# Performance work log

Measured on AMD Instinct MI355X. Metric: run time of the kernel, lower is better.

Reference implementation:

```python
import jax, jax.numpy as jnp
import numpy as np

B, S, D, H, E, K = 2, 2048, 1024, 2048, 8, 2


def setup_inputs() -> dict:
    key = jax.random.key(0)
    ks = jax.random.split(key, 9)
    sc_d = 1.0 / np.sqrt(D)
    sc_h = 1.0 / np.sqrt(H)
    return {
        "x": jax.random.normal(ks[0], (B, S, D), dtype=jnp.float32),
        "w_router": jax.random.normal(ks[1], (E, D), dtype=jnp.float32) * sc_d,
        "Wg": jax.random.normal(ks[2], (E, H, D), dtype=jnp.float32) * sc_d,  # per-expert gate proj (torch Linear weight layout [out,in])
        "Wu": jax.random.normal(ks[3], (E, H, D), dtype=jnp.float32) * sc_d,
        "Wd": jax.random.normal(ks[4], (E, D, H), dtype=jnp.float32) * sc_h,
        "sg": jax.random.normal(ks[5], (H, D), dtype=jnp.float32) * sc_d,  # shared expert
        "su": jax.random.normal(ks[6], (H, D), dtype=jnp.float32) * sc_d,
        "sd": jax.random.normal(ks[7], (D, H), dtype=jnp.float32) * sc_h,
    }


def reference(x, w_router, Wg, Wu, Wd, sg, su, sd):
    b, s, d = x.shape
    xf = x.reshape(-1, d)  # [T, D]

    # --- gating ---
    logits = jnp.einsum("td,ed->te", xf, w_router)
    probs = jax.nn.softmax(logits, axis=-1)  # [T, E]
    topw, topi = jax.lax.top_k(probs, K)  # [T, K]
    topw = topw / jnp.sum(topw, axis=-1, keepdims=True)
    # combine weights per (token, expert): topk indices are distinct per token
    comb = jnp.sum(topw[..., None] * jax.nn.one_hot(topi, E, dtype=xf.dtype), axis=1)  # [T, E]

    # --- shared expert (SwiGLU) ---
    shared = jnp.einsum(
        "th,dh->td",
        jax.nn.silu(jnp.einsum("td,hd->th", xf, sg)) * jnp.einsum("td,hd->th", xf, su),
        sd,
    )

    # --- routed experts: dense all-expert compute, weighted combine ---
    h1 = jax.nn.silu(jnp.einsum("td,ehd->teh", xf, Wg))
    h2 = jnp.einsum("td,ehd->teh", xf, Wu)
    eo = jnp.einsum("teh,edh->ted", h1 * h2, Wd)  # [T, E, D]
    routed = jnp.einsum("te,ted->td", comb, eo)

    return (routed + shared).reshape(b, s, d)
```

## Files before the change

kernel.cpp:

```cpp
#include <hip/hip_runtime.h>
#include <hip/hip_bf16.h>

#define T_TOK 4096
#define D_DIM 1024
#define H_DIM 2048

typedef __attribute__((ext_vector_type(8))) short short8;
typedef __attribute__((ext_vector_type(8))) unsigned short ushort8;
typedef __attribute__((ext_vector_type(4))) float floatx4;

__device__ __forceinline__ unsigned short f2bf(float f) {
  unsigned int u = __builtin_bit_cast(unsigned int, f);
  return (unsigned short)((u + 0x7fffu + ((u >> 16) & 1u)) >> 16);
}

__device__ __forceinline__ float bf2f(unsigned short s) {
  unsigned int u = ((unsigned int)s) << 16;
  return __builtin_bit_cast(float, u);
}

__device__ __forceinline__ void glds16(const ushort* g, ushort* l) {
  __builtin_amdgcn_global_load_lds(
      (const __attribute__((address_space(1))) unsigned int*)g,
      (__attribute__((address_space(3))) unsigned int*)l, 16, 0, 0);
}

__global__ void prep_kernel(const float4* __restrict__ Wg, ushort4* __restrict__ Wgb,
                            const float4* __restrict__ Wu, ushort4* __restrict__ Wub,
                            const float4* __restrict__ Wd, ushort4* __restrict__ Wdb,
                            const float4* __restrict__ sg, ushort4* __restrict__ sgb,
                            const float4* __restrict__ su, ushort4* __restrict__ sub,
                            const float4* __restrict__ sd, ushort4* __restrict__ sdb,
                            const float* __restrict__ x, const float* __restrict__ wr,
                            ushort* __restrict__ xb,
                            int* __restrict__ topi, float2* __restrict__ topw) {
  if (blockIdx.x < 27648) {
    int i2 = (blockIdx.x * 256 + threadIdx.x) * 2;
    const float4* s; ushort4* d; int i;
    if (i2 < 4194304)       { s = Wg; d = Wgb; i = i2; }
    else if (i2 < 8388608)  { s = Wu; d = Wub; i = i2 - 4194304; }
    else if (i2 < 12582912) { s = Wd; d = Wdb; i = i2 - 8388608; }
    else if (i2 < 13107200) { s = sg; d = sgb; i = i2 - 12582912; }
    else if (i2 < 13631488) { s = su; d = sub; i = i2 - 13107200; }
    else                    { s = sd; d = sdb; i = i2 - 13631488; }
    float4 v0 = s[i];
    float4 v1 = s[i + 1];
    ushort8 o;
    o[0] = f2bf(v0.x); o[1] = f2bf(v0.y); o[2] = f2bf(v0.z); o[3] = f2bf(v0.w);
    o[4] = f2bf(v1.x); o[5] = f2bf(v1.y); o[6] = f2bf(v1.z); o[7] = f2bf(v1.w);
    *(ushort8*)(d + i) = o;
    return;
  }
  const int w = threadIdx.x >> 6;
  const int l = threadIdx.x & 63;
  const int t = (blockIdx.x - 27648) * 4 + w;
  const float4* xr = (const float4*)(x + (size_t)t * D_DIM);
  ushort4* xo = (ushort4*)(xb + (size_t)t * D_DIM);
  float p[8];
#pragma unroll
  for (int e = 0; e < 8; ++e) p[e] = 0.f;
#pragma unroll
  for (int i = 0; i < 4; ++i) {
    float4 xv = xr[i * 64 + l];
    ushort4 o;
    o.x = f2bf(xv.x); o.y = f2bf(xv.y); o.z = f2bf(xv.z); o.w = f2bf(xv.w);
    xo[i * 64 + l] = o;
#pragma unroll
    for (int e = 0; e < 8; ++e) {
      float4 wv = ((const float4*)(wr + e * D_DIM))[i * 64 + l];
      p[e] += xv.x * wv.x + xv.y * wv.y + xv.z * wv.z + xv.w * wv.w;
    }
  }
#pragma unroll
  for (int off = 32; off > 0; off >>= 1) {
#pragma unroll
    for (int e = 0; e < 8; ++e) p[e] += __shfl_xor(p[e], off, 64);
  }
  if (l == 0) {
    float mx = p[0];
#pragma unroll
    for (int e = 1; e < 8; ++e) mx = fmaxf(mx, p[e]);
    float pr[8];
#pragma unroll
    for (int e = 0; e < 8; ++e) pr[e] = __expf(p[e] - mx);
    int i0 = 0;
#pragma unroll
    for (int e = 1; e < 8; ++e) if (pr[e] > pr[i0]) i0 = e;
    int i1 = (i0 == 0) ? 1 : 0;
#pragma unroll
    for (int e = 0; e < 8; ++e) if (e != i0 && pr[e] > pr[i1]) i1 = e;
    float w0 = pr[i0], w1 = pr[i1];
    float inv = 1.f / (w0 + w1);
    topi[t] = i0 | (i1 << 8);
    topw[t] = make_float2(w0 * inv, w1 * inv);
  }
}

__global__ void build_lists_kernel(const int* __restrict__ topi,
                                   int* __restrict__ counts, int* __restrict__ list,
                                   int* __restrict__ pos) {
  const int e = blockIdx.x;
  const int tid = threadIdx.x;
  const int l = tid & 63;
  const int w = tid >> 6;
  __shared__ int wtot[4];
  int base = 0;
  for (int c = 0; c < T_TOK; c += 256) {
    int t = c + tid;
    int ti = topi[t];
    int e0 = ti & 255, e1 = ti >> 8;
    bool flag = (e0 == e) || (e1 == e);
    unsigned long long m = __ballot(flag);
    int lanepos = __popcll(m & ((1ull << l) - 1ull));
    if (l == 0) wtot[w] = __popcll(m);
    __syncthreads();
    int waveoff = 0;
#pragma unroll
    for (int i = 0; i < 4; ++i) waveoff += (i < w) ? wtot[i] : 0;
    int tot = wtot[0] + wtot[1] + wtot[2] + wtot[3];
    if (flag) {
      int p = base + waveoff + lanepos;
      list[e * T_TOK + p] = t;
      int slot = (e0 == e) ? 0 : 1;
      pos[t * 2 + slot] = p;
    }
    base += tot;
    __syncthreads();
  }
  if (tid == 0) counts[e] = base;
}

__global__ __launch_bounds__(256, 2)
void gemm1_kernel(const ushort* __restrict__ xb,
                  const ushort* __restrict__ Wgb, const ushort* __restrict__ Wub,
                  const ushort* __restrict__ sgb, const ushort* __restrict__ sub,
                  const int* __restrict__ list, const int* __restrict__ counts,
                  ushort* __restrict__ h) {
  const int e = blockIdx.z;
  int n_e, hbase;
  {
    int acc = 0, ce = 0;
    for (int q = 0; q < 8; ++q) {
      int c = counts[q];
      if (q < e) acc += c;
      if (q == e) ce = c;
    }
    n_e = (e == 8) ? T_TOK : ce;
    hbase = (e == 8) ? 8192 : acc;
  }
  const int r0 = blockIdx.y * 128;
  if (r0 >= n_e) return;
  const int c0 = blockIdx.x * 128;
  const ushort* Wg = (e == 8) ? sgb : (Wgb + (size_t)e * H_DIM * D_DIM);
  const ushort* Wu = (e == 8) ? sub : (Wub + (size_t)e * H_DIM * D_DIM);
  const int hrow0 = hbase + r0;

  __shared__ __align__(16) ushort As[128 * 64];
  __shared__ __align__(16) ushort Bgs[128 * 64];
  __shared__ __align__(16) ushort Bus[128 * 64];
  __shared__ int toks[128];

  const int tid = threadIdx.x;
  const int l = tid & 63;
  const int w = tid >> 6;

  if (tid < 128) {
    int rr = r0 + tid;
    toks[tid] = (e == 8) ? ((rr < T_TOK) ? rr : (T_TOK - 1))
                         : list[e * T_TOK + ((rr < n_e) ? rr : (n_e - 1))];
  }
  __syncthreads();

  const int lrow8 = l >> 3;
  const int csw = (((l & 7) ^ lrow8) << 3);
  const ushort* ap[4];
#pragma unroll
  for (int i = 0; i < 4; ++i) {
    int ri = (w * 4 + i) * 8 + lrow8;
    ap[i] = xb + (size_t)toks[ri] * D_DIM + csw;
  }
  const ushort* bgp = Wg + (size_t)(c0 + w * 32 + lrow8) * D_DIM + csw;
  const ushort* bup = Wu + (size_t)(c0 + w * 32 + lrow8) * D_DIM + csw;

  floatx4 accg[4][4], accu[4][4];
#pragma unroll
  for (int i = 0; i < 4; ++i)
#pragma unroll
    for (int j = 0; j < 4; ++j) {
      accg[i][j] = (floatx4)(0.f);
      accu[i][j] = (floatx4)(0.f);
    }

  const int mrow = (w & 1) * 64;
  const int ncol = (w >> 1) * 64;
  int rba[4], rbb[4];
#pragma unroll
  for (int i = 0; i < 4; ++i) {
    rba[i] = (mrow + 16 * i + (l & 15)) * 64;
    rbb[i] = (ncol + 16 * i + (l & 15)) * 64;
  }

  for (int k0 = 0; k0 < D_DIM; k0 += 64) {
    __syncthreads();
#pragma unroll
    for (int i = 0; i < 4; ++i) {
      glds16(ap[i] + k0,                As  + (w * 4 + i) * 512);
      glds16(bgp + k0 + i * 8 * D_DIM,  Bgs + (w * 4 + i) * 512);
      glds16(bup + k0 + i * 8 * D_DIM,  Bus + (w * 4 + i) * 512);
    }
    __syncthreads();
#pragma unroll
    for (int s = 0; s < 2; ++s) {
      const int pq = ((((s << 2) | (l >> 4)) ^ (l & 7)) << 3);
      short8 a[4], bg[4], bu[4];
#pragma unroll
      for (int i = 0; i < 4; ++i) a[i] = *(const short8*)(As + rba[i] + pq);
#pragma unroll
      for (int j = 0; j < 4; ++j) {
        bg[j] = *(const short8*)(Bgs + rbb[j] + pq);
        bu[j] = *(const short8*)(Bus + rbb[j] + pq);
      }
#pragma unroll
      for (int i = 0; i < 4; ++i)
#pragma unroll
        for (int j = 0; j < 4; ++j) {
          accg[i][j] = __builtin_amdgcn_mfma_f32_16x16x32_bf16(a[i], bg[j], accg[i][j], 0, 0, 0);
          accu[i][j] = __builtin_amdgcn_mfma_f32_16x16x32_bf16(a[i], bu[j], accu[i][j], 0, 0, 0);
        }
    }
  }

#pragma unroll
  for (int i = 0; i < 4; ++i) {
#pragma unroll
    for (int r = 0; r < 4; ++r) {
      int lrow = mrow + 16 * i + (l >> 4) * 4 + r;
      if (r0 + lrow < n_e) {
#pragma unroll
        for (int j = 0; j < 4; ++j) {
          float g = accg[i][j][r];
          float u = accu[i][j][r];
          float hv = (g / (1.f + __expf(-g))) * u;
          int col = c0 + ncol + 16 * j + (l & 15);
          h[(size_t)(hrow0 + lrow) * H_DIM + col] = f2bf(hv);
        }
      }
    }
  }
}

__global__ __launch_bounds__(256, 2)
void gemm2_kernel(const ushort* __restrict__ h,
                  const ushort* __restrict__ Wdb, const ushort* __restrict__ sdb,
                  const int* __restrict__ counts,
                  ushort* __restrict__ eo) {
  const int e = blockIdx.z;
  int n_e, hbase;
  {
    int acc = 0, ce = 0;
    for (int q = 0; q < 8; ++q) {
      int c = counts[q];
      if (q < e) acc += c;
      if (q == e) ce = c;
    }
    n_e = (e == 8) ? T_TOK : ce;
    hbase = (e == 8) ? 8192 : acc;
  }
  const int r0 = blockIdx.y * 128;
  if (r0 >= n_e) return;
  const int c0 = blockIdx.x * 256;
  const ushort* Wd = (e == 8) ? sdb : (Wdb + (size_t)e * D_DIM * H_DIM);
  const int hrow0 = hbase + r0;

  __shared__ __align__(16) ushort As[128 * 64];
  __shared__ __align__(16) ushort Bs[256 * 64];

  const int tid = threadIdx.x;
  const int l = tid & 63;
  const int w = tid >> 6;

  const int lrow8 = l >> 3;
  const int csw = (((l & 7) ^ lrow8) << 3);
  const ushort* apb = h  + (size_t)(hrow0 + w * 32 + lrow8) * H_DIM + csw;
  const ushort* bpb = Wd + (size_t)(c0 + w * 64 + lrow8) * H_DIM + csw;

  floatx4 acc[4][8];
#pragma unroll
  for (int i = 0; i < 4; ++i)
#pragma unroll
    for (int j = 0; j < 8; ++j) acc[i][j] = (floatx4)(0.f);

  const int mrow = (w & 1) * 64;
  const int ncol = (w >> 1) * 128;
  int rba[4], rbb[8];
#pragma unroll
  for (int i = 0; i < 4; ++i) rba[i] = (mrow + 16 * i + (l & 15)) * 64;
#pragma unroll
  for (int j = 0; j < 8; ++j) rbb[j] = (ncol + 16 * j + (l & 15)) * 64;

  for (int k0 = 0; k0 < H_DIM; k0 += 64) {
    __syncthreads();
#pragma unroll
    for (int i = 0; i < 4; ++i)
      glds16(apb + k0 + i * 8 * H_DIM, As + (w * 4 + i) * 512);
#pragma unroll
    for (int i = 0; i < 8; ++i)
      glds16(bpb + k0 + i * 8 * H_DIM, Bs + (w * 8 + i) * 512);
    __syncthreads();
#pragma unroll
    for (int s = 0; s < 2; ++s) {
      const int pq = ((((s << 2) | (l >> 4)) ^ (l & 7)) << 3);
      short8 a[4], b[8];
#pragma unroll
      for (int i = 0; i < 4; ++i) a[i] = *(const short8*)(As + rba[i] + pq);
#pragma unroll
      for (int j = 0; j < 8; ++j) b[j] = *(const short8*)(Bs + rbb[j] + pq);
#pragma unroll
      for (int i = 0; i < 4; ++i)
#pragma unroll
        for (int j = 0; j < 8; ++j)
          acc[i][j] = __builtin_amdgcn_mfma_f32_16x16x32_bf16(a[i], b[j], acc[i][j], 0, 0, 0);
    }
  }

#pragma unroll
  for (int i = 0; i < 4; ++i) {
#pragma unroll
    for (int r = 0; r < 4; ++r) {
      int lrow = mrow + 16 * i + (l >> 4) * 4 + r;
      if (r0 + lrow < n_e) {
#pragma unroll
        for (int j = 0; j < 8; ++j) {
          int col = c0 + ncol + 16 * j + (l & 15);
          eo[(size_t)(hrow0 + lrow) * D_DIM + col] = f2bf(acc[i][j][r]);
        }
      }
    }
  }
}

__global__ void combine_kernel(const ushort* __restrict__ eo, const int* __restrict__ topi,
                               const float2* __restrict__ topw, const int* __restrict__ pos,
                               const int* __restrict__ counts, float* __restrict__ out) {
  const int t = blockIdx.x * 2 + (threadIdx.x >> 7);
  const int c = threadIdx.x & 127;
  int ti = topi[t];
  int e0 = ti & 255, e1 = ti >> 8;
  int off0 = 0, off1 = 0;
#pragma unroll
  for (int q = 0; q < 8; ++q) {
    int cc = counts[q];
    off0 += (q < e0) ? cc : 0;
    off1 += (q < e1) ? cc : 0;
  }
  float2 wv = topw[t];
  int2 p = ((const int2*)pos)[t];
  const short8* ra = (const short8*)(eo + (size_t)(off0 + p.x) * D_DIM);
  const short8* rb = (const short8*)(eo + (size_t)(off1 + p.y) * D_DIM);
  const short8* rs = (const short8*)(eo + (size_t)(8192 + t) * D_DIM);
  short8 a = ra[c], b = rb[c], s = rs[c];
  float o[8];
#pragma unroll
  for (int j = 0; j < 8; ++j)
    o[j] = wv.x * bf2f((unsigned short)a[j]) + wv.y * bf2f((unsigned short)b[j]) +
           bf2f((unsigned short)s[j]);
  float4* op = (float4*)(out + (size_t)t * D_DIM + c * 8);
  op[0] = make_float4(o[0], o[1], o[2], o[3]);
  op[1] = make_float4(o[4], o[5], o[6], o[7]);
}

#define OFF_XB   0ull
#define OFF_WGB  (OFF_XB + 8388608ull)
#define OFF_WUB  (OFF_WGB + 33554432ull)
#define OFF_WDB  (OFF_WUB + 33554432ull)
#define OFF_SGB  (OFF_WDB + 33554432ull)
#define OFF_SUB  (OFF_SGB + 4194304ull)
#define OFF_SDB  (OFF_SUB + 4194304ull)
#define OFF_H    (OFF_SDB + 4194304ull)
#define OFF_EO   OFF_WGB
#define OFF_CNT  (OFF_H + 50331648ull)
#define OFF_LIST (OFF_CNT + 64ull)
#define OFF_POS  (OFF_LIST + 131072ull)
#define OFF_TOPI (OFF_POS + 32768ull)
#define OFF_TOPW (OFF_TOPI + 16384ull)

extern "C" void kernel_launch(void* const* d_in, const int* in_sizes, int n_in,
                              void* d_out, int out_size, void* d_ws, size_t ws_size,
                              hipStream_t stream) {
  const float* x  = (const float*)d_in[0];
  const float* wr = (const float*)d_in[1];
  const float* Wg = (const float*)d_in[2];
  const float* Wu = (const float*)d_in[3];
  const float* Wd = (const float*)d_in[4];
  const float* sg = (const float*)d_in[5];
  const float* su = (const float*)d_in[6];
  const float* sd = (const float*)d_in[7];
  float* out = (float*)d_out;
  char* ws = (char*)d_ws;

  ushort* xb  = (ushort*)(ws + OFF_XB);
  ushort* Wgb = (ushort*)(ws + OFF_WGB);
  ushort* Wub = (ushort*)(ws + OFF_WUB);
  ushort* Wdb = (ushort*)(ws + OFF_WDB);
  ushort* sgb = (ushort*)(ws + OFF_SGB);
  ushort* sub = (ushort*)(ws + OFF_SUB);
  ushort* sdb = (ushort*)(ws + OFF_SDB);
  ushort* hbuf = (ushort*)(ws + OFF_H);
  ushort* eo   = (ushort*)(ws + OFF_EO);
  int* counts = (int*)(ws + OFF_CNT);
  int* list   = (int*)(ws + OFF_LIST);
  int* pos    = (int*)(ws + OFF_POS);
  int* topi   = (int*)(ws + OFF_TOPI);
  float2* topw = (float2*)(ws + OFF_TOPW);

  prep_kernel<<<28672, 256, 0, stream>>>((const float4*)Wg, (ushort4*)Wgb,
                                         (const float4*)Wu, (ushort4*)Wub,
                                         (const float4*)Wd, (ushort4*)Wdb,
                                         (const float4*)sg, (ushort4*)sgb,
                                         (const float4*)su, (ushort4*)sub,
                                         (const float4*)sd, (ushort4*)sdb,
                                         x, wr, xb, topi, topw);
  build_lists_kernel<<<8, 256, 0, stream>>>(topi, counts, list, pos);

  gemm1_kernel<<<dim3(16, 32, 9), 256, 0, stream>>>(xb, Wgb, Wub, sgb, sub,
                                                    list, counts, hbuf);
  gemm2_kernel<<<dim3(4, 32, 9), 256, 0, stream>>>(hbuf, Wdb, sdb, counts, eo);
  combine_kernel<<<2048, 256, 0, stream>>>(eo, topi, topw, pos, counts, out);
}
```

Before: 452.8 us.

## Overlap Wd/sd bf16 conversion with gemm1 and shrink gemm2 tile width

```diff
diff --git a/kernel.cpp b/kernel.cpp
--- a/kernel.cpp
+++ b/kernel.cpp
@@ -27,22 +27,19 @@
 
 __global__ void prep_kernel(const float4* __restrict__ Wg, ushort4* __restrict__ Wgb,
                             const float4* __restrict__ Wu, ushort4* __restrict__ Wub,
-                            const float4* __restrict__ Wd, ushort4* __restrict__ Wdb,
                             const float4* __restrict__ sg, ushort4* __restrict__ sgb,
                             const float4* __restrict__ su, ushort4* __restrict__ sub,
-                            const float4* __restrict__ sd, ushort4* __restrict__ sdb,
                             const float* __restrict__ x, const float* __restrict__ wr,
                             ushort* __restrict__ xb,
                             int* __restrict__ topi, float2* __restrict__ topw) {
-  if (blockIdx.x < 27648) {
-    int i2 = (blockIdx.x * 256 + threadIdx.x) * 2;
-    const float4* s; ushort4* d; int i;
-    if (i2 < 4194304)       { s = Wg; d = Wgb; i = i2; }
-    else if (i2 < 8388608)  { s = Wu; d = Wub; i = i2 - 4194304; }
-    else if (i2 < 12582912) { s = Wd; d = Wdb; i = i2 - 8388608; }
-    else if (i2 < 13107200) { s = sg; d = sgb; i = i2 - 12582912; }
-    else if (i2 < 13631488) { s = su; d = sub; i = i2 - 13107200; }
-    else                    { s = sd; d = sdb; i = i2 - 13631488; }
+  if (blockIdx.x < 18432) {
+    int p = blockIdx.x * 256 + threadIdx.x;
+    const float4* s; ushort4* d; int pp;
+    if (p < 2097152)      { s = Wg; d = Wgb; pp = p; }
+    else if (p < 4194304) { s = Wu; d = Wub; pp = p - 2097152; }
+    else if (p < 4456448) { s = sg; d = sgb; pp = p - 4194304; }
+    else                  { s = su; d = sub; pp = p - 4456448; }
+    int i = pp * 2;
     float4 v0 = s[i];
     float4 v1 = s[i + 1];
     ushort8 o;
@@ -53,7 +50,7 @@
   }
   const int w = threadIdx.x >> 6;
   const int l = threadIdx.x & 63;
-  const int t = (blockIdx.x - 27648) * 4 + w;
+  const int t = (blockIdx.x - 18432) * 4 + w;
   const float4* xr = (const float4*)(x + (size_t)t * D_DIM);
   ushort4* xo = (ushort4*)(xb + (size_t)t * D_DIM);
   float p[8];
@@ -135,8 +132,33 @@
                   const ushort* __restrict__ Wgb, const ushort* __restrict__ Wub,
                   const ushort* __restrict__ sgb, const ushort* __restrict__ sub,
                   const int* __restrict__ list, const int* __restrict__ counts,
-                  ushort* __restrict__ h) {
-  const int e = blockIdx.z;
+                  ushort* __restrict__ h,
+                  const float4* __restrict__ Wd32, ushort4* __restrict__ Wdb,
+                  const float4* __restrict__ sd32, ushort4* __restrict__ sdb) {
+  const int hlin = blockIdx.x;
+  if ((hlin % 10) == 9) {
+    int base = (hlin / 10) * 256 + threadIdx.x;
+#pragma unroll
+    for (int it = 0; it < 18; ++it) {
+      int p = base + it * 131072;
+      const float4* s; ushort4* d; int i;
+      if (p < 2097152) { s = Wd32; d = Wdb; i = p * 2; }
+      else             { s = sd32; d = sdb; i = (p - 2097152) * 2; }
+      float4 v0 = s[i];
+      float4 v1 = s[i + 1];
+      ushort8 o;
+      o[0] = f2bf(v0.x); o[1] = f2bf(v0.y); o[2] = f2bf(v0.z); o[3] = f2bf(v0.w);
+      o[4] = f2bf(v1.x); o[5] = f2bf(v1.y); o[6] = f2bf(v1.z); o[7] = f2bf(v1.w);
+      *(ushort8*)(d + i) = o;
+    }
+    return;
+  }
+  const int g = hlin - (hlin + 1) / 10;
+  const int e = g >> 9;
+  const int rem = g & 511;
+  const int by = rem >> 4;
+  const int bx = rem & 15;
+
   int n_e, hbase;
   {
     int acc = 0, ce = 0;
@@ -148,9 +170,9 @@
     n_e = (e == 8) ? T_TOK : ce;
     hbase = (e == 8) ? 8192 : acc;
   }
-  const int r0 = blockIdx.y * 128;
+  const int r0 = by * 128;
   if (r0 >= n_e) return;
-  const int c0 = blockIdx.x * 128;
+  const int c0 = bx * 128;
   const ushort* Wg = (e == 8) ? sgb : (Wgb + (size_t)e * H_DIM * D_DIM);
   const ushort* Wu = (e == 8) ? sub : (Wub + (size_t)e * H_DIM * D_DIM);
   const int hrow0 = hbase + r0;
@@ -238,9 +260,9 @@
       if (r0 + lrow < n_e) {
 #pragma unroll
         for (int j = 0; j < 4; ++j) {
-          float g = accg[i][j][r];
+          float g2 = accg[i][j][r];
           float u = accu[i][j][r];
-          float hv = (g / (1.f + __expf(-g))) * u;
+          float hv = (g2 / (1.f + __expf(-g2))) * u;
           int col = c0 + ncol + 16 * j + (l & 15);
           h[(size_t)(hrow0 + lrow) * H_DIM + col] = f2bf(hv);
         }
@@ -257,23 +279,23 @@
   const int e = blockIdx.z;
   int n_e, hbase;
   {
-    int acc = 0, ce = 0;
+    int acc0 = 0, ce = 0;
     for (int q = 0; q < 8; ++q) {
       int c = counts[q];
-      if (q < e) acc += c;
+      if (q < e) acc0 += c;
       if (q == e) ce = c;
     }
     n_e = (e == 8) ? T_TOK : ce;
-    hbase = (e == 8) ? 8192 : acc;
+    hbase = (e == 8) ? 8192 : acc0;
   }
   const int r0 = blockIdx.y * 128;
   if (r0 >= n_e) return;
-  const int c0 = blockIdx.x * 256;
+  const int c0 = blockIdx.x * 128;
   const ushort* Wd = (e == 8) ? sdb : (Wdb + (size_t)e * D_DIM * H_DIM);
   const int hrow0 = hbase + r0;
 
   __shared__ __align__(16) ushort As[128 * 64];
-  __shared__ __align__(16) ushort Bs[256 * 64];
+  __shared__ __align__(16) ushort Bs[128 * 64];
 
   const int tid = threadIdx.x;
   const int l = tid & 63;
@@ -282,43 +304,43 @@
   const int lrow8 = l >> 3;
   const int csw = (((l & 7) ^ lrow8) << 3);
   const ushort* apb = h  + (size_t)(hrow0 + w * 32 + lrow8) * H_DIM + csw;
-  const ushort* bpb = Wd + (size_t)(c0 + w * 64 + lrow8) * H_DIM + csw;
-
-  floatx4 acc[4][8];
+  const ushort* bpb = Wd + (size_t)(c0 + w * 32 + lrow8) * H_DIM + csw;
+
+  floatx4 acc[4][4];
 #pragma unroll
   for (int i = 0; i < 4; ++i)
 #pragma unroll
-    for (int j = 0; j < 8; ++j) acc[i][j] = (floatx4)(0.f);
+    for (int j = 0; j < 4; ++j) acc[i][j] = (floatx4)(0.f);
 
   const int mrow = (w & 1) * 64;
-  const int ncol = (w >> 1) * 128;
-  int rba[4], rbb[8];
-#pragma unroll
-  for (int i = 0; i < 4; ++i) rba[i] = (mrow + 16 * i + (l & 15)) * 64;
-#pragma unroll
-  for (int j = 0; j < 8; ++j) rbb[j] = (ncol + 16 * j + (l & 15)) * 64;
+  const int ncol = (w >> 1) * 64;
+  int rba[4], rbb[4];
+#pragma unroll
+  for (int i = 0; i < 4; ++i) {
+    rba[i] = (mrow + 16 * i + (l & 15)) * 64;
+    rbb[i] = (ncol + 16 * i + (l & 15)) * 64;
+  }
 
   for (int k0 = 0; k0 < H_DIM; k0 += 64) {
     __syncthreads();
 #pragma unroll
-    for (int i = 0; i < 4; ++i)
+    for (int i = 0; i < 4; ++i) {
       glds16(apb + k0 + i * 8 * H_DIM, As + (w * 4 + i) * 512);
-#pragma unroll
-    for (int i = 0; i < 8; ++i)
-      glds16(bpb + k0 + i * 8 * H_DIM, Bs + (w * 8 + i) * 512);
+      glds16(bpb + k0 + i * 8 * H_DIM, Bs + (w * 4 + i) * 512);
+    }
     __syncthreads();
 #pragma unroll
     for (int s = 0; s < 2; ++s) {
       const int pq = ((((s << 2) | (l >> 4)) ^ (l & 7)) << 3);
-      short8 a[4], b[8];
+      short8 a[4], b[4];
 #pragma unroll
       for (int i = 0; i < 4; ++i) a[i] = *(const short8*)(As + rba[i] + pq);
 #pragma unroll
-      for (int j = 0; j < 8; ++j) b[j] = *(const short8*)(Bs + rbb[j] + pq);
+      for (int j = 0; j < 4; ++j) b[j] = *(const short8*)(Bs + rbb[j] + pq);
 #pragma unroll
       for (int i = 0; i < 4; ++i)
 #pragma unroll
-        for (int j = 0; j < 8; ++j)
+        for (int j = 0; j < 4; ++j)
           acc[i][j] = __builtin_amdgcn_mfma_f32_16x16x32_bf16(a[i], b[j], acc[i][j], 0, 0, 0);
     }
   }
@@ -330,7 +352,7 @@
       int lrow = mrow + 16 * i + (l >> 4) * 4 + r;
       if (r0 + lrow < n_e) {
 #pragma unroll
-        for (int j = 0; j < 8; ++j) {
+        for (int j = 0; j < 4; ++j) {
           int col = c0 + ncol + 16 * j + (l & 15);
           eo[(size_t)(hrow0 + lrow) * D_DIM + col] = f2bf(acc[i][j][r]);
         }
@@ -413,17 +435,17 @@
   int* topi   = (int*)(ws + OFF_TOPI);
   float2* topw = (float2*)(ws + OFF_TOPW);
 
-  prep_kernel<<<28672, 256, 0, stream>>>((const float4*)Wg, (ushort4*)Wgb,
+  prep_kernel<<<19456, 256, 0, stream>>>((const float4*)Wg, (ushort4*)Wgb,
                                          (const float4*)Wu, (ushort4*)Wub,
-                                         (const float4*)Wd, (ushort4*)Wdb,
                                          (const float4*)sg, (ushort4*)sgb,
                                          (const float4*)su, (ushort4*)sub,
-                                         (const float4*)sd, (ushort4*)sdb,
                                          x, wr, xb, topi, topw);
   build_lists_kernel<<<8, 256, 0, stream>>>(topi, counts, list, pos);
 
-  gemm1_kernel<<<dim3(16, 32, 9), 256, 0, stream>>>(xb, Wgb, Wub, sgb, sub,
-                                                    list, counts, hbuf);
-  gemm2_kernel<<<dim3(4, 32, 9), 256, 0, stream>>>(hbuf, Wdb, sdb, counts, eo);
+  gemm1_kernel<<<5120, 256, 0, stream>>>(xb, Wgb, Wub, sgb, sub,
+                                         list, counts, hbuf,
+                                         (const float4*)Wd, (ushort4*)Wdb,
+                                         (const float4*)sd, (ushort4*)sdb);
+  gemm2_kernel<<<dim3(8, 32, 9), 256, 0, stream>>>(hbuf, Wdb, sdb, counts, eo);
   combine_kernel<<<2048, 256, 0, stream>>>(eo, topi, topw, pos, counts, out);
 }
```

New measurement: 474.8 us. +4.9%, slower.

## Split router into own kernel and overlap list build with weight conversion

Applied to the files above, without the earlier changes.

```diff
diff --git a/kernel.cpp b/kernel.cpp
--- a/kernel.cpp
+++ b/kernel.cpp
@@ -25,35 +25,12 @@
       (__attribute__((address_space(3))) unsigned int*)l, 16, 0, 0);
 }
 
-__global__ void prep_kernel(const float4* __restrict__ Wg, ushort4* __restrict__ Wgb,
-                            const float4* __restrict__ Wu, ushort4* __restrict__ Wub,
-                            const float4* __restrict__ Wd, ushort4* __restrict__ Wdb,
-                            const float4* __restrict__ sg, ushort4* __restrict__ sgb,
-                            const float4* __restrict__ su, ushort4* __restrict__ sub,
-                            const float4* __restrict__ sd, ushort4* __restrict__ sdb,
-                            const float* __restrict__ x, const float* __restrict__ wr,
-                            ushort* __restrict__ xb,
-                            int* __restrict__ topi, float2* __restrict__ topw) {
-  if (blockIdx.x < 27648) {
-    int i2 = (blockIdx.x * 256 + threadIdx.x) * 2;
-    const float4* s; ushort4* d; int i;
-    if (i2 < 4194304)       { s = Wg; d = Wgb; i = i2; }
-    else if (i2 < 8388608)  { s = Wu; d = Wub; i = i2 - 4194304; }
-    else if (i2 < 12582912) { s = Wd; d = Wdb; i = i2 - 8388608; }
-    else if (i2 < 13107200) { s = sg; d = sgb; i = i2 - 12582912; }
-    else if (i2 < 13631488) { s = su; d = sub; i = i2 - 13107200; }
-    else                    { s = sd; d = sdb; i = i2 - 13631488; }
-    float4 v0 = s[i];
-    float4 v1 = s[i + 1];
-    ushort8 o;
-    o[0] = f2bf(v0.x); o[1] = f2bf(v0.y); o[2] = f2bf(v0.z); o[3] = f2bf(v0.w);
-    o[4] = f2bf(v1.x); o[5] = f2bf(v1.y); o[6] = f2bf(v1.z); o[7] = f2bf(v1.w);
-    *(ushort8*)(d + i) = o;
-    return;
-  }
+__global__ void router_kernel(const float* __restrict__ x, const float* __restrict__ wr,
+                              ushort* __restrict__ xb,
+                              int* __restrict__ topi, float2* __restrict__ topw) {
   const int w = threadIdx.x >> 6;
   const int l = threadIdx.x & 63;
-  const int t = (blockIdx.x - 27648) * 4 + w;
+  const int t = blockIdx.x * 4 + w;
   const float4* xr = (const float4*)(x + (size_t)t * D_DIM);
   ushort4* xo = (ushort4*)(xb + (size_t)t * D_DIM);
   float p[8];
@@ -96,9 +73,30 @@
   }
 }
 
-__global__ void build_lists_kernel(const int* __restrict__ topi,
-                                   int* __restrict__ counts, int* __restrict__ list,
-                                   int* __restrict__ pos) {
+__global__ void cvt_build_kernel(const float4* __restrict__ Wg, ushort4* __restrict__ Wgb,
+                                 const float4* __restrict__ Wu, ushort4* __restrict__ Wub,
+                                 const float4* __restrict__ Wd, ushort4* __restrict__ Wdb,
+                                 const float4* __restrict__ sg, ushort4* __restrict__ sgb,
+                                 const float4* __restrict__ su, ushort4* __restrict__ sub,
+                                 const float4* __restrict__ sd, ushort4* __restrict__ sdb,
+                                 const int* __restrict__ topi,
+                                 int* __restrict__ counts, int* __restrict__ list,
+                                 int* __restrict__ pos) {
+  if (blockIdx.x >= 8) {
+    int id = (blockIdx.x - 8) * 256 + threadIdx.x;
+    const float4* s; ushort4* d; int i;
+    if (id < 4194304)       { s = Wg; d = Wgb; i = id; }
+    else if (id < 8388608)  { s = Wu; d = Wub; i = id - 4194304; }
+    else if (id < 12582912) { s = Wd; d = Wdb; i = id - 8388608; }
+    else if (id < 13107200) { s = sg; d = sgb; i = id - 12582912; }
+    else if (id < 13631488) { s = su; d = sub; i = id - 13107200; }
+    else                    { s = sd; d = sdb; i = id - 13631488; }
+    float4 v = s[i];
+    ushort4 o;
+    o.x = f2bf(v.x); o.y = f2bf(v.y); o.z = f2bf(v.z); o.w = f2bf(v.w);
+    d[i] = o;
+    return;
+  }
   const int e = blockIdx.x;
   const int tid = threadIdx.x;
   const int l = tid & 63;
@@ -413,14 +411,14 @@
   int* topi   = (int*)(ws + OFF_TOPI);
   float2* topw = (float2*)(ws + OFF_TOPW);
 
-  prep_kernel<<<28672, 256, 0, stream>>>((const float4*)Wg, (ushort4*)Wgb,
-                                         (const float4*)Wu, (ushort4*)Wub,
-                                         (const float4*)Wd, (ushort4*)Wdb,
-                                         (const float4*)sg, (ushort4*)sgb,
-                                         (const float4*)su, (ushort4*)sub,
-                                         (const float4*)sd, (ushort4*)sdb,
-                                         x, wr, xb, topi, topw);
-  build_lists_kernel<<<8, 256, 0, stream>>>(topi, counts, list, pos);
+  router_kernel<<<1024, 256, 0, stream>>>(x, wr, xb, topi, topw);
+  cvt_build_kernel<<<55304, 256, 0, stream>>>((const float4*)Wg, (ushort4*)Wgb,
+                                              (const float4*)Wu, (ushort4*)Wub,
+                                              (const float4*)Wd, (ushort4*)Wdb,
+                                              (const float4*)sg, (ushort4*)sgb,
+                                              (const float4*)su, (ushort4*)sub,
+                                              (const float4*)sd, (ushort4*)sdb,
+                                              topi, counts, list, pos);
 
   gemm1_kernel<<<dim3(16, 32, 9), 256, 0, stream>>>(xb, Wgb, Wub, sgb, sub,
                                                     list, counts, hbuf);
```

Result: faster. 435.4 us (median of 2 runs) (-3.8%).
